# Performance work log

Hardware: AMD Instinct MI355X
Metric: run time of the kernel (lower is better)

Reference implementation:

```python
import jax, jax.numpy as jnp
import numpy as np

N_HEAD = 16

def setup_inputs() -> dict:
    key = jax.random.key(0)
    k1, k2, k3, k4, k5 = jax.random.split(key, 5)
    B, T, C = 2, 2048, 1024
    x = jax.random.normal(k1, (B, T, C), dtype=jnp.float32)
    s = 0.02
    W_attn = jax.random.normal(k2, (C, 3 * C), dtype=jnp.float32) * s
    b_attn = jnp.zeros((3 * C,), dtype=jnp.float32)
    W_proj = jax.random.normal(k3, (C, C), dtype=jnp.float32) * s
    b_proj = jnp.zeros((C,), dtype=jnp.float32)
    return {"x": x, "W_attn": W_attn, "b_attn": b_attn, "W_proj": W_proj, "b_proj": b_proj}

def reference(x, W_attn, b_attn, W_proj, b_proj):
    B, T, C = x.shape
    H = N_HEAD
    hd = C // H
    qkv = x @ W_attn + b_attn                      # (B,T,3C)
    q, k, v = jnp.split(qkv, 3, axis=-1)
    # (B,T,C) -> (B,H,T,hd)
    def to_heads(t):
        return t.reshape(B, T, H, hd).transpose(0, 2, 1, 3)
    q, k, v = to_heads(q), to_heads(k), to_heads(v)
    scale = 1.0 / jnp.sqrt(jnp.asarray(hd, dtype=x.dtype))
    att = jnp.einsum('bhqd,bhkd->bhqk', q, k) * scale  # (B,H,T,T)
    causal = jnp.tril(jnp.ones((T, T), dtype=bool))
    att = jnp.where(causal[None, None], att, -jnp.inf)
    att = jax.nn.softmax(att, axis=-1)
    y = jnp.einsum('bhqk,bhkd->bhqd', att, v)          # (B,H,T,hd)
    y = y.transpose(0, 2, 1, 3).reshape(B, T, C)
    return y @ W_proj + b_proj
```

## Files before the change

kernel.cpp:

```cpp
#include <hip/hip_runtime.h>

#define N_HEAD 16

typedef __attribute__((ext_vector_type(8))) __bf16 bf16x8;
typedef __attribute__((ext_vector_type(8))) short  s16x8;
typedef __attribute__((ext_vector_type(4))) short  s16x4;
typedef __attribute__((ext_vector_type(4))) float  f32x4;
typedef __attribute__((ext_vector_type(4))) unsigned u32x4;

#if __has_builtin(__builtin_amdgcn_exp2f)
#define EXP2(x) __builtin_amdgcn_exp2f(x)
#else
#define EXP2(x) exp2f(x)
#endif
#if __has_builtin(__builtin_amdgcn_rcpf)
#define RCP(x) __builtin_amdgcn_rcpf(x)
#else
#define RCP(x) (1.0f / (x))
#endif

static __device__ __forceinline__ short f2bf(float f) {
    unsigned u = __builtin_bit_cast(unsigned, f);
    unsigned r = (u + 0x7FFFu + ((u >> 16) & 1u)) >> 16;
    return (short)r;
}

static __device__ __forceinline__ unsigned cvt_pk_bf16(float lo, float hi) {
    unsigned d;
    asm("v_cvt_pk_bf16_f32 %0, %1, %2" : "=v"(d) : "v"(lo), "v"(hi));
    return d;
}

static __device__ __forceinline__ void gload_lds16(const void* g, void* l) {
    __builtin_amdgcn_global_load_lds(
        (const __attribute__((address_space(1))) void*)g,
        (__attribute__((address_space(3))) void*)l, 16, 0, 0);
}

__global__ __launch_bounds__(256) void cvt_bf16(
    const float* __restrict__ X, short* __restrict__ Y, int n)
{
    int idx = blockIdx.x * 256 + threadIdx.x;
    size_t base = (size_t)idx * 8;
    if (base + 8 > (size_t)n) return;
    float4 f0 = *(const float4*)&X[base];
    float4 f1 = *(const float4*)&X[base + 4];
    s16x8 o;
    o[0] = f2bf(f0.x); o[1] = f2bf(f0.y); o[2] = f2bf(f0.z); o[3] = f2bf(f0.w);
    o[4] = f2bf(f1.x); o[5] = f2bf(f1.y); o[6] = f2bf(f1.z); o[7] = f2bf(f1.w);
    *(s16x8*)&Y[base] = o;
}

__global__ __launch_bounds__(256) void transpose_w(
    const float* __restrict__ W, short* __restrict__ Wt, int N, int K)
{
    __shared__ short Ts[64][72];
    const int n0 = blockIdx.x * 64, k0 = blockIdx.y * 64;
    const int tid = threadIdx.x;
    const int r = tid >> 4, c4 = (tid & 15) * 4;
#pragma unroll
    for (int i = 0; i < 4; ++i) {
        int row = r + i * 16;
        float4 f = *(const float4*)&W[(size_t)(k0 + row) * N + n0 + c4];
        s16x4 s = { f2bf(f.x), f2bf(f.y), f2bf(f.z), f2bf(f.w) };
        *(s16x4*)&Ts[row][c4] = s;
    }
    __syncthreads();
#pragma unroll
    for (int i = 0; i < 4; ++i) {
        int row = r + i * 16;
        s16x4 s = { Ts[c4 + 0][row], Ts[c4 + 1][row], Ts[c4 + 2][row], Ts[c4 + 3][row] };
        *(s16x4*)&Wt[(size_t)(n0 + row) * K + k0 + c4] = s;
    }
}

__global__ __launch_bounds__(256) void qkv_gemm(
    const short* __restrict__ Xb,
    const short* __restrict__ Wt,
    const float* __restrict__ bias,
    short* __restrict__ Qo, short* __restrict__ Ko, short* __restrict__ Vo)
{
    __shared__ short As[2][128 * 32];
    __shared__ short Bs[2][128 * 32];
    const int tid = threadIdx.x, wave = tid >> 6, lane = tid & 63;
    const int row0 = blockIdx.x * 128, col0 = blockIdx.y * 128;
    const int srow = wave * 16 + (lane >> 2);
    const int scol = (lane & 3) * 8;
    const short* aS = Xb + (size_t)(row0 + srow) * 1024 + scol;
    const short* bS = Wt + (size_t)(col0 + srow) * 1024 + scol;
    const int woff = wave * 512;
    const int wr = (wave >> 1) * 64, wc = (wave & 1) * 64;
    const int arow = lane & 15, ksub = (lane >> 4) * 8;

    f32x4 acc[4][4] = {};

    gload_lds16(aS,             As[0] + woff);
    gload_lds16(aS + 64 * 1024, As[0] + woff + 2048);
    gload_lds16(bS,             Bs[0] + woff);
    gload_lds16(bS + 64 * 1024, Bs[0] + woff + 2048);
    __syncthreads();

    int cur = 0;
    for (int k0 = 0; k0 < 1024; k0 += 32) {
        if (k0 + 32 < 1024) {
            gload_lds16(aS + k0 + 32,             As[cur ^ 1] + woff);
            gload_lds16(aS + k0 + 32 + 64 * 1024, As[cur ^ 1] + woff + 2048);
            gload_lds16(bS + k0 + 32,             Bs[cur ^ 1] + woff);
            gload_lds16(bS + k0 + 32 + 64 * 1024, Bs[cur ^ 1] + woff + 2048);
        }
        bf16x8 af[4], bfr[4];
#pragma unroll
        for (int i = 0; i < 4; ++i) af[i]  = *(const bf16x8*)&As[cur][(wr + i * 16 + arow) * 32 + ksub];
#pragma unroll
        for (int j = 0; j < 4; ++j) bfr[j] = *(const bf16x8*)&Bs[cur][(wc + j * 16 + arow) * 32 + ksub];
#pragma unroll
        for (int i = 0; i < 4; ++i)
#pragma unroll
            for (int j = 0; j < 4; ++j)
                acc[i][j] = __builtin_amdgcn_mfma_f32_16x16x32_bf16(af[i], bfr[j], acc[i][j], 0, 0, 0);
        __syncthreads();
        cur ^= 1;
    }

    const int ccol = lane & 15, crow = (lane >> 4) * 4;
#pragma unroll
    for (int i = 0; i < 4; ++i)
#pragma unroll
        for (int j = 0; j < 4; ++j)
#pragma unroll
            for (int r = 0; r < 4; ++r) {
                int m = row0 + wr + i * 16 + crow + r;
                int n = col0 + wc + j * 16 + ccol;
                float val = acc[i][j][r] + bias[n];
                int which = n >> 10;
                int nc = n & 1023;
                int head = nc >> 6, hd = nc & 63;
                int b = m >> 11, t = m & 2047;
                if (which == 0) {
                    Qo[((size_t)(b * N_HEAD + head) * 2048 + t) * 64 + hd] = f2bf(val * 0.18033688f);
                } else if (which == 1) {
                    Ko[((size_t)(b * N_HEAD + head) * 2048 + t) * 64 + hd] = f2bf(val);
                } else {
                    Vo[((size_t)(b * N_HEAD + head) * 64 + hd) * 2048 + t] = f2bf(val);
                }
            }
}

__global__ __launch_bounds__(256) void attn_kernel(
    const short* __restrict__ Q, const short* __restrict__ K,
    const short* __restrict__ Vt, short* __restrict__ Y)
{
    __shared__ short Ks[2][64 * 64];
    __shared__ short Vs[2][64 * 64];
    const int bh = blockIdx.x;
    const int qt = gridDim.y - 1 - blockIdx.y;
    const int q0 = qt * 64;
    const int b = bh >> 4, h = bh & 15;
    const short* Qh = Q  + (size_t)bh * 2048 * 64;
    const short* Kh = K  + (size_t)bh * 2048 * 64;
    const short* Vh = Vt + (size_t)bh * 64 * 2048;
    const int tid = threadIdx.x, wave = tid >> 6, lane = tid & 63;
    const int qrow0 = q0 + wave * 16;
    const int arow = lane & 15, g = lane >> 4;

    const int rho = wave * 16 + (lane >> 3);
    const int kappa = ((rho >> 5) << 5) | (((rho >> 2) & 3) << 3)
                    | (((rho >> 4) & 1) << 2) | (rho & 3);
    const int xchunk = 8 * ((lane & 7) ^ (rho & 7));
    const short* kSrc = Kh + (size_t)kappa * 64 + xchunk;
    const short* vSrc = Vh + (size_t)rho * 2048 + xchunk;

    bf16x8 qfr[2];
#pragma unroll
    for (int c = 0; c < 2; ++c)
        qfr[c] = *(const bf16x8*)&Qh[(size_t)(qrow0 + arow) * 64 + c * 32 + (g * 8)];

    f32x4 o[4] = {};
    float lsum = 0.f;

    const int nt = qt + 1;

    gload_lds16(kSrc,            Ks[0] + wave * 1024);
    gload_lds16(kSrc + 1024,     Ks[0] + wave * 1024 + 512);
    gload_lds16(vSrc,            Vs[0] + wave * 1024);
    gload_lds16(vSrc + 8 * 2048, Vs[0] + wave * 1024 + 512);
    __syncthreads();

    int cur = 0;
    for (int t = 0; t < nt; ++t) {
        const int kt = t << 6;
        if (t + 1 < nt) {
            const int kn = kt + 64;
            short* kD = Ks[cur ^ 1] + wave * 1024;
            short* vD = Vs[cur ^ 1] + wave * 1024;
            gload_lds16(kSrc + (size_t)kn * 64,        kD);
            gload_lds16(kSrc + (size_t)kn * 64 + 1024, kD + 512);
            gload_lds16(vSrc + kn,                     vD);
            gload_lds16(vSrc + kn + 8 * 2048,          vD + 512);
        }
        if (kt <= qrow0 + 15) {
            const short* Kc = Ks[cur];
            const short* Vc = Vs[cur];
            const bool need_mask = (kt + 64) > qrow0;
            f32x4 s[4] = {};
#pragma unroll
            for (int kc = 0; kc < 4; ++kc) {
                int krow = kc * 16 + arow;
                int xr = krow & 7;
#pragma unroll
                for (int c = 0; c < 2; ++c) {
                    bf16x8 kf = *(const bf16x8*)&Kc[krow * 64 + (((c * 4 + g) ^ xr) * 8)];
                    s[kc] = __builtin_amdgcn_mfma_f32_16x16x32_bf16(kf, qfr[c], s[kc], 0, 0, 0);
                }
            }
            if (need_mask) {
                int q = qrow0 + arow;
#pragma unroll
                for (int kc = 0; kc < 4; ++kc) {
                    int keyb = kt + ((kc >> 1) << 5) + (g << 3) + ((kc & 1) << 2);
#pragma unroll
                    for (int r = 0; r < 4; ++r)
                        if (keyb + r > q) s[kc][r] = -3.0e38f;
                }
            }
            unsigned pa[8];
#pragma unroll
            for (int kc = 0; kc < 4; ++kc) {
                float p0 = EXP2(s[kc][0]);
                float p1 = EXP2(s[kc][1]);
                float p2 = EXP2(s[kc][2]);
                float p3 = EXP2(s[kc][3]);
                lsum += (p0 + p1) + (p2 + p3);
                pa[kc * 2 + 0] = cvt_pk_bf16(p0, p1);
                pa[kc * 2 + 1] = cvt_pk_bf16(p2, p3);
            }
#pragma unroll
            for (int c = 0; c < 2; ++c) {
                bf16x8 pb = __builtin_bit_cast(bf16x8,
                    (u32x4){ pa[4 * c], pa[4 * c + 1], pa[4 * c + 2], pa[4 * c + 3] });
#pragma unroll
                for (int j = 0; j < 4; ++j) {
                    int d = j * 16 + arow;
                    bf16x8 vf = *(const bf16x8*)&Vc[d * 64 + (((c * 4 + g) ^ (d & 7)) * 8)];
                    o[j] = __builtin_amdgcn_mfma_f32_16x16x32_bf16(vf, pb, o[j], 0, 0, 0);
                }
            }
        }
        __syncthreads();
        cur ^= 1;
    }

    {
        float l = lsum;
        l += __shfl_xor(l, 16);
        l += __shfl_xor(l, 32);
        float li = RCP(l);
        int t = qrow0 + arow;
#pragma unroll
        for (int j = 0; j < 4; ++j) {
            s16x4 ov = { f2bf(o[j][0] * li), f2bf(o[j][1] * li),
                         f2bf(o[j][2] * li), f2bf(o[j][3] * li) };
            *(s16x4*)&Y[((size_t)(b * 2048 + t)) * 1024 + h * 64 + j * 16 + 4 * g] = ov;
        }
    }
}

__global__ __launch_bounds__(256) void proj_gemm(
    const short* __restrict__ Yb,
    const short* __restrict__ Wpt,
    const float* __restrict__ bias,
    float* __restrict__ Out)
{
    __shared__ short As[2][128 * 32];
    __shared__ short Bs[2][128 * 32];
    const int tid = threadIdx.x, wave = tid >> 6, lane = tid & 63;
    const int row0 = blockIdx.x * 128, col0 = blockIdx.y * 128;
    const int srow = wave * 16 + (lane >> 2);
    const int scol = (lane & 3) * 8;
    const short* aS = Yb  + (size_t)(row0 + srow) * 1024 + scol;
    const short* bS = Wpt + (size_t)(col0 + srow) * 1024 + scol;
    const int woff = wave * 512;
    const int wr = (wave >> 1) * 64, wc = (wave & 1) * 64;
    const int arow = lane & 15, ksub = (lane >> 4) * 8;

    f32x4 acc[4][4] = {};

    gload_lds16(aS,             As[0] + woff);
    gload_lds16(aS + 64 * 1024, As[0] + woff + 2048);
    gload_lds16(bS,             Bs[0] + woff);
    gload_lds16(bS + 64 * 1024, Bs[0] + woff + 2048);
    __syncthreads();

    int cur = 0;
    for (int k0 = 0; k0 < 1024; k0 += 32) {
        if (k0 + 32 < 1024) {
            gload_lds16(aS + k0 + 32,             As[cur ^ 1] + woff);
            gload_lds16(aS + k0 + 32 + 64 * 1024, As[cur ^ 1] + woff + 2048);
            gload_lds16(bS + k0 + 32,             Bs[cur ^ 1] + woff);
            gload_lds16(bS + k0 + 32 + 64 * 1024, Bs[cur ^ 1] + woff + 2048);
        }
        bf16x8 af[4], bfr[4];
#pragma unroll
        for (int i = 0; i < 4; ++i) af[i]  = *(const bf16x8*)&As[cur][(wr + i * 16 + arow) * 32 + ksub];
#pragma unroll
        for (int j = 0; j < 4; ++j) bfr[j] = *(const bf16x8*)&Bs[cur][(wc + j * 16 + arow) * 32 + ksub];
#pragma unroll
        for (int i = 0; i < 4; ++i)
#pragma unroll
            for (int j = 0; j < 4; ++j)
                acc[i][j] = __builtin_amdgcn_mfma_f32_16x16x32_bf16(af[i], bfr[j], acc[i][j], 0, 0, 0);
        __syncthreads();
        cur ^= 1;
    }

    const int ccol = lane & 15, crow = (lane >> 4) * 4;
#pragma unroll
    for (int i = 0; i < 4; ++i)
#pragma unroll
        for (int j = 0; j < 4; ++j)
#pragma unroll
            for (int r = 0; r < 4; ++r) {
                int m = row0 + wr + i * 16 + crow + r;
                int n = col0 + wc + j * 16 + ccol;
                Out[(size_t)m * 1024 + n] = acc[i][j][r] + bias[n];
            }
}

extern "C" void kernel_launch(void* const* d_in, const int* in_sizes, int n_in,
                              void* d_out, int out_size, void* d_ws, size_t ws_size,
                              hipStream_t stream) {
    const float* x      = (const float*)d_in[0];
    const float* W_attn = (const float*)d_in[1];
    const float* b_attn = (const float*)d_in[2];
    const float* W_proj = (const float*)d_in[3];
    const float* b_proj = (const float*)d_in[4];
    float* out = (float*)d_out;

    short* Xb  = (short*)d_ws;
    short* Wat = Xb + 4194304;
    short* Wpt = Wat + 3145728;
    short* qb  = Wpt + 1048576;
    short* kb  = qb + 4194304;
    short* vb  = kb + 4194304;
    short* yb  = Xb;

    cvt_bf16<<<2048, 256, 0, stream>>>(x, Xb, 4194304);
    transpose_w<<<dim3(48, 16), 256, 0, stream>>>(W_attn, Wat, 3072, 1024);
    transpose_w<<<dim3(16, 16), 256, 0, stream>>>(W_proj, Wpt, 1024, 1024);
    qkv_gemm<<<dim3(32, 24), 256, 0, stream>>>(Xb, Wat, b_attn, qb, kb, vb);
    attn_kernel<<<dim3(32, 32), 256, 0, stream>>>(qb, kb, vb, yb);
    proj_gemm<<<dim3(32, 8), 256, 0, stream>>>(yb, Wpt, b_proj, out);
}
```

Baseline: 115.0 us.

## Rewrite QKV GEMM as 256x256 tile, 8-wave pipelined kernel with swizzled LDS

The QKV projection GEMM now uses 512-thread blocks computing 256x256 output tiles with K-step 64. Global-to-LDS loads are issued in staged quarters interleaved with MFMA phases under explicit barriers, vmcnt waits and s_setprio, and LDS columns are XOR-swizzled to avoid bank conflicts. Block IDs are remapped for L2 locality and the V store is vectorized. This aims at more data reuse and better overlap of memory and compute, at the cost of larger LDS use, high register pressure and a grid of only 192 blocks.

```diff
diff --git a/kernel.cpp b/kernel.cpp
--- a/kernel.cpp
+++ b/kernel.cpp
@@ -36,6 +36,11 @@
         (const __attribute__((address_space(1))) void*)g,
         (__attribute__((address_space(3))) void*)l, 16, 0, 0);
 }
+
+#define BARX() do { asm volatile("" ::: "memory"); __builtin_amdgcn_s_barrier(); \
+                    asm volatile("" ::: "memory"); } while (0)
+#define VMCNT4() asm volatile("s_waitcnt vmcnt(4)" ::: "memory")
+#define VMCNT0() asm volatile("s_waitcnt vmcnt(0)" ::: "memory")
 
 __global__ __launch_bounds__(256) void cvt_bf16(
     const float* __restrict__ X, short* __restrict__ Y, int n)
@@ -74,76 +79,137 @@
     }
 }
 
-__global__ __launch_bounds__(256) void qkv_gemm(
+__global__ __launch_bounds__(512, 1) void qkv_gemm(
     const short* __restrict__ Xb,
     const short* __restrict__ Wt,
     const float* __restrict__ bias,
     short* __restrict__ Qo, short* __restrict__ Ko, short* __restrict__ Vo)
 {
-    __shared__ short As[2][128 * 32];
-    __shared__ short Bs[2][128 * 32];
+    __shared__ short As[2][2][8192];
+    __shared__ short Bs[2][2][8192];
     const int tid = threadIdx.x, wave = tid >> 6, lane = tid & 63;
-    const int row0 = blockIdx.x * 128, col0 = blockIdx.y * 128;
-    const int srow = wave * 16 + (lane >> 2);
-    const int scol = (lane & 3) * 8;
-    const short* aS = Xb + (size_t)(row0 + srow) * 1024 + scol;
-    const short* bS = Wt + (size_t)(col0 + srow) * 1024 + scol;
-    const int woff = wave * 512;
-    const int wr = (wave >> 1) * 64, wc = (wave & 1) * 64;
-    const int arow = lane & 15, ksub = (lane >> 4) * 8;
-
-    f32x4 acc[4][4] = {};
-
-    gload_lds16(aS,             As[0] + woff);
-    gload_lds16(aS + 64 * 1024, As[0] + woff + 2048);
-    gload_lds16(bS,             Bs[0] + woff);
-    gload_lds16(bS + 64 * 1024, Bs[0] + woff + 2048);
-    __syncthreads();
-
-    int cur = 0;
-    for (int k0 = 0; k0 < 1024; k0 += 32) {
-        if (k0 + 32 < 1024) {
-            gload_lds16(aS + k0 + 32,             As[cur ^ 1] + woff);
-            gload_lds16(aS + k0 + 32 + 64 * 1024, As[cur ^ 1] + woff + 2048);
-            gload_lds16(bS + k0 + 32,             Bs[cur ^ 1] + woff);
-            gload_lds16(bS + k0 + 32 + 64 * 1024, Bs[cur ^ 1] + woff + 2048);
-        }
-        bf16x8 af[4], bfr[4];
-#pragma unroll
-        for (int i = 0; i < 4; ++i) af[i]  = *(const bf16x8*)&As[cur][(wr + i * 16 + arow) * 32 + ksub];
-#pragma unroll
-        for (int j = 0; j < 4; ++j) bfr[j] = *(const bf16x8*)&Bs[cur][(wc + j * 16 + arow) * 32 + ksub];
-#pragma unroll
-        for (int i = 0; i < 4; ++i)
-#pragma unroll
-            for (int j = 0; j < 4; ++j)
-                acc[i][j] = __builtin_amdgcn_mfma_f32_16x16x32_bf16(af[i], bfr[j], acc[i][j], 0, 0, 0);
-        __syncthreads();
-        cur ^= 1;
-    }
-
-    const int ccol = lane & 15, crow = (lane >> 4) * 4;
-#pragma unroll
-    for (int i = 0; i < 4; ++i)
-#pragma unroll
-        for (int j = 0; j < 4; ++j)
-#pragma unroll
-            for (int r = 0; r < 4; ++r) {
-                int m = row0 + wr + i * 16 + crow + r;
-                int n = col0 + wc + j * 16 + ccol;
-                float val = acc[i][j][r] + bias[n];
-                int which = n >> 10;
-                int nc = n & 1023;
-                int head = nc >> 6, hd = nc & 63;
-                int b = m >> 11, t = m & 2047;
-                if (which == 0) {
-                    Qo[((size_t)(b * N_HEAD + head) * 2048 + t) * 64 + hd] = f2bf(val * 0.18033688f);
-                } else if (which == 1) {
-                    Ko[((size_t)(b * N_HEAD + head) * 2048 + t) * 64 + hd] = f2bf(val);
-                } else {
-                    Vo[((size_t)(b * N_HEAD + head) * 64 + hd) * 2048 + t] = f2bf(val);
-                }
-            }
+    int bidf = blockIdx.y * 16 + blockIdx.x;
+    bidf = (bidf & 7) * 24 + (bidf >> 3);
+    const int row0 = (bidf % 16) * 256, col0 = (bidf / 16) * 256;
+    const int wm = wave >> 2, wn = wave & 3;
+    const int arow = lane & 15, g = lane >> 4;
+    const int xsw = (arow & 4) << 2;
+    const int aoff0 = (g * 8) ^ xsw;
+    const int aoff1 = (g * 8 + 32) ^ xsw;
+
+    const int srow = tid >> 3;
+    const int sc = ((tid & 7) * 8) ^ (((srow >> 2) & 1) << 4);
+    const short* aBase = Xb + (size_t)(row0 + srow) * 1024 + sc;
+    const short* bBase = Wt + (size_t)(col0 + srow) * 1024 + sc;
+    short* aD = &As[0][0][0] + wave * 512;
+    short* bD = &Bs[0][0][0] + wave * 512;
+
+#define STAGE(t, s) do { const int _b = ((t) & 1) * 16384; const size_t _k = (size_t)(t) * 64; \
+    if ((s) == 0)      { gload_lds16(aBase + _k,          aD + _b);         gload_lds16(aBase + _k + 65536,  aD + _b + 4096); } \
+    else if ((s) == 3) { gload_lds16(aBase + _k + 131072, aD + _b + 8192);  gload_lds16(aBase + _k + 196608, aD + _b + 12288); } \
+    else if ((s) == 1) { gload_lds16(bBase + _k,          bD + _b);         gload_lds16(bBase + _k + 65536,  bD + _b + 4096); } \
+    else               { gload_lds16(bBase + _k + 131072, bD + _b + 8192);  gload_lds16(bBase + _k + 196608, bD + _b + 12288); } \
+} while (0)
+
+    bf16x8 af[4][2], bfr[2][2][2];
+    f32x4 acc[8][4] = {};
+
+#define LDA8(BUF, MH) do { const short* _p = &As[BUF][wm][(MH) * 4096 + arow * 64]; \
+    af[0][0] = *(const bf16x8*)(_p + aoff0);        af[0][1] = *(const bf16x8*)(_p + aoff1); \
+    af[1][0] = *(const bf16x8*)(_p + 1024 + aoff0); af[1][1] = *(const bf16x8*)(_p + 1024 + aoff1); \
+    af[2][0] = *(const bf16x8*)(_p + 2048 + aoff0); af[2][1] = *(const bf16x8*)(_p + 2048 + aoff1); \
+    af[3][0] = *(const bf16x8*)(_p + 3072 + aoff0); af[3][1] = *(const bf16x8*)(_p + 3072 + aoff1); \
+} while (0)
+
+#define LDB4(BUF, NH) do { const short* _p = &Bs[BUF][wn >> 1][(wn & 1) * 4096 + (NH) * 2048 + arow * 64]; \
+    bfr[NH][0][0] = *(const bf16x8*)(_p + aoff0);        bfr[NH][0][1] = *(const bf16x8*)(_p + aoff1); \
+    bfr[NH][1][0] = *(const bf16x8*)(_p + 1024 + aoff0); bfr[NH][1][1] = *(const bf16x8*)(_p + 1024 + aoff1); \
+} while (0)
+
+#define MM(MH, NH, mm, nn) do { \
+    acc[(MH)*4+mm][(NH)*2+nn] = __builtin_amdgcn_mfma_f32_16x16x32_bf16(af[mm][0], bfr[NH][nn][0], acc[(MH)*4+mm][(NH)*2+nn], 0, 0, 0); \
+    acc[(MH)*4+mm][(NH)*2+nn] = __builtin_amdgcn_mfma_f32_16x16x32_bf16(af[mm][1], bfr[NH][nn][1], acc[(MH)*4+mm][(NH)*2+nn], 0, 0, 0); \
+} while (0)
+#define MF16(MH, NH) do { MM(MH,NH,0,0); MM(MH,NH,0,1); MM(MH,NH,1,0); MM(MH,NH,1,1); \
+                          MM(MH,NH,2,0); MM(MH,NH,2,1); MM(MH,NH,3,0); MM(MH,NH,3,1); } while (0)
+
+#define PRIO1() __builtin_amdgcn_s_setprio(1)
+#define PRIO0() __builtin_amdgcn_s_setprio(0)
+
+#define HALFPH(BUF, STa, STb, STc, STd, VM) do { \
+    LDA8(BUF, 0); LDB4(BUF, 0); STa; BARX(); \
+    PRIO1(); MF16(0, 0); PRIO0(); BARX(); \
+    LDB4(BUF, 1); STb; BARX(); \
+    PRIO1(); MF16(0, 1); PRIO0(); BARX(); \
+    LDA8(BUF, 1); STc; BARX(); \
+    PRIO1(); MF16(1, 1); PRIO0(); BARX(); \
+    STd; VM; BARX(); \
+    PRIO1(); MF16(1, 0); PRIO0(); BARX(); \
+} while (0)
+
+    STAGE(0, 0); STAGE(0, 1); STAGE(0, 2); STAGE(0, 3);
+    STAGE(1, 1); STAGE(1, 2);
+    VMCNT4(); BARX();
+
+    for (int i = 0; i < 7; ++i) {
+        HALFPH(0, STAGE(2*i+1, 0), STAGE(2*i+1, 3), STAGE(2*i+2, 1), STAGE(2*i+2, 2), VMCNT4());
+        HALFPH(1, STAGE(2*i+2, 0), STAGE(2*i+2, 3), STAGE(2*i+3, 1), STAGE(2*i+3, 2), VMCNT4());
+    }
+    HALFPH(0, STAGE(15, 0), STAGE(15, 3), ((void)0), ((void)0), VMCNT0());
+    HALFPH(1, ((void)0), ((void)0), ((void)0), ((void)0), VMCNT0());
+
+    const int which = col0 >> 10;
+    const int bb = row0 >> 11;
+    const int nc0 = (col0 & 1023) + wn * 64 + arow;
+    const int t0 = (row0 & 2047) + wm * 128 + g * 4;
+    float bv[4];
+#pragma unroll
+    for (int n = 0; n < 4; ++n) bv[n] = bias[col0 + wn * 64 + n * 16 + arow];
+
+    if (which == 0) {
+#pragma unroll
+        for (int n = 0; n < 4; ++n) {
+            int nc = nc0 + n * 16, head = nc >> 6, hd = nc & 63;
+#pragma unroll
+            for (int m = 0; m < 8; ++m) {
+                size_t tb = (size_t)(bb * N_HEAD + head) * 2048 + t0 + m * 16;
+#pragma unroll
+                for (int r = 0; r < 4; ++r)
+                    Qo[(tb + r) * 64 + hd] = f2bf((acc[m][n][r] + bv[n]) * 0.18033688f);
+            }
+        }
+    } else if (which == 1) {
+#pragma unroll
+        for (int n = 0; n < 4; ++n) {
+            int nc = nc0 + n * 16, head = nc >> 6, hd = nc & 63;
+#pragma unroll
+            for (int m = 0; m < 8; ++m) {
+                size_t tb = (size_t)(bb * N_HEAD + head) * 2048 + t0 + m * 16;
+#pragma unroll
+                for (int r = 0; r < 4; ++r)
+                    Ko[(tb + r) * 64 + hd] = f2bf(acc[m][n][r] + bv[n]);
+            }
+        }
+    } else {
+#pragma unroll
+        for (int n = 0; n < 4; ++n) {
+            int nc = nc0 + n * 16, head = nc >> 6, hd = nc & 63;
+#pragma unroll
+            for (int m = 0; m < 8; ++m) {
+                s16x4 ov = { f2bf(acc[m][n][0] + bv[n]), f2bf(acc[m][n][1] + bv[n]),
+                             f2bf(acc[m][n][2] + bv[n]), f2bf(acc[m][n][3] + bv[n]) };
+                *(s16x4*)&Vo[((size_t)(bb * N_HEAD + head) * 64 + hd) * 2048 + t0 + m * 16] = ov;
+            }
+        }
+    }
+#undef STAGE
+#undef LDA8
+#undef LDB4
+#undef MM
+#undef MF16
+#undef HALFPH
+#undef PRIO1
+#undef PRIO0
 }
 
 __global__ __launch_bounds__(256) void attn_kernel(
@@ -271,8 +337,8 @@
     const float* __restrict__ bias,
     float* __restrict__ Out)
 {
-    __shared__ short As[2][128 * 32];
-    __shared__ short Bs[2][128 * 32];
+    __shared__ short As2[2][128 * 32];
+    __shared__ short Bs2[2][128 * 32];
     const int tid = threadIdx.x, wave = tid >> 6, lane = tid & 63;
     const int row0 = blockIdx.x * 128, col0 = blockIdx.y * 128;
     const int srow = wave * 16 + (lane >> 2);
@@ -285,25 +351,25 @@
 
     f32x4 acc[4][4] = {};
 
-    gload_lds16(aS,             As[0] + woff);
-    gload_lds16(aS + 64 * 1024, As[0] + woff + 2048);
-    gload_lds16(bS,             Bs[0] + woff);
-    gload_lds16(bS + 64 * 1024, Bs[0] + woff + 2048);
+    gload_lds16(aS,             As2[0] + woff);
+    gload_lds16(aS + 64 * 1024, As2[0] + woff + 2048);
+    gload_lds16(bS,             Bs2[0] + woff);
+    gload_lds16(bS + 64 * 1024, Bs2[0] + woff + 2048);
     __syncthreads();
 
     int cur = 0;
     for (int k0 = 0; k0 < 1024; k0 += 32) {
         if (k0 + 32 < 1024) {
-            gload_lds16(aS + k0 + 32,             As[cur ^ 1] + woff);
-            gload_lds16(aS + k0 + 32 + 64 * 1024, As[cur ^ 1] + woff + 2048);
-            gload_lds16(bS + k0 + 32,             Bs[cur ^ 1] + woff);
-            gload_lds16(bS + k0 + 32 + 64 * 1024, Bs[cur ^ 1] + woff + 2048);
+            gload_lds16(aS + k0 + 32,             As2[cur ^ 1] + woff);
+            gload_lds16(aS + k0 + 32 + 64 * 1024, As2[cur ^ 1] + woff + 2048);
+            gload_lds16(bS + k0 + 32,             Bs2[cur ^ 1] + woff);
+            gload_lds16(bS + k0 + 32 + 64 * 1024, Bs2[cur ^ 1] + woff + 2048);
         }
         bf16x8 af[4], bfr[4];
 #pragma unroll
-        for (int i = 0; i < 4; ++i) af[i]  = *(const bf16x8*)&As[cur][(wr + i * 16 + arow) * 32 + ksub];
-#pragma unroll
-        for (int j = 0; j < 4; ++j) bfr[j] = *(const bf16x8*)&Bs[cur][(wc + j * 16 + arow) * 32 + ksub];
+        for (int i = 0; i < 4; ++i) af[i]  = *(const bf16x8*)&As2[cur][(wr + i * 16 + arow) * 32 + ksub];
+#pragma unroll
+        for (int j = 0; j < 4; ++j) bfr[j] = *(const bf16x8*)&Bs2[cur][(wc + j * 16 + arow) * 32 + ksub];
 #pragma unroll
         for (int i = 0; i < 4; ++i)
 #pragma unroll
@@ -347,7 +413,7 @@
     cvt_bf16<<<2048, 256, 0, stream>>>(x, Xb, 4194304);
     transpose_w<<<dim3(48, 16), 256, 0, stream>>>(W_attn, Wat, 3072, 1024);
     transpose_w<<<dim3(16, 16), 256, 0, stream>>>(W_proj, Wpt, 1024, 1024);
-    qkv_gemm<<<dim3(32, 24), 256, 0, stream>>>(Xb, Wat, b_attn, qb, kb, vb);
+    qkv_gemm<<<dim3(16, 12), 512, 0, stream>>>(Xb, Wat, b_attn, qb, kb, vb);
     attn_kernel<<<dim3(32, 32), 256, 0, stream>>>(qb, kb, vb, yb);
     proj_gemm<<<dim3(32, 8), 256, 0, stream>>>(yb, Wpt, b_proj, out);
 }
```

New measurement: 118.0 us. +2.7%, slower.

## Triple-buffer GEMM LDS staging with swizzled layout and vmcnt-based waits

Applied to the files above, without the earlier changes.

Both GEMM kernels move from double to triple buffering, keeping two tiles in flight and waiting with explicit s_waitcnt vmcnt(4) plus a raw barrier instead of a full __syncthreads drain. The K-chunk position within each LDS row is XOR-swizzled on the global-to-LDS copy and matched on the fragment reads, to reduce LDS bank conflicts. The QKV epilogue hoists the Q/K/V choice and bias load out of the inner loops and writes V in 4-element vector stores. LDS use grows by half, which may lower occupancy, and correctness depends on the hand-counted vmcnt values.

```diff
diff --git a/kernel.cpp b/kernel.cpp
--- a/kernel.cpp
+++ b/kernel.cpp
@@ -37,6 +37,11 @@
         (__attribute__((address_space(3))) void*)l, 16, 0, 0);
 }
 
+#define BARX() do { asm volatile("" ::: "memory"); __builtin_amdgcn_s_barrier(); \
+                    asm volatile("" ::: "memory"); } while (0)
+#define VMCNT4() asm volatile("s_waitcnt vmcnt(4)" ::: "memory")
+#define VMCNT0() asm volatile("s_waitcnt vmcnt(0)" ::: "memory")
+
 __global__ __launch_bounds__(256) void cvt_bf16(
     const float* __restrict__ X, short* __restrict__ Y, int n)
 {
@@ -80,70 +85,94 @@
     const float* __restrict__ bias,
     short* __restrict__ Qo, short* __restrict__ Ko, short* __restrict__ Vo)
 {
-    __shared__ short As[2][128 * 32];
-    __shared__ short Bs[2][128 * 32];
+    __shared__ short As[3 * 4096];
+    __shared__ short Bs[3 * 4096];
     const int tid = threadIdx.x, wave = tid >> 6, lane = tid & 63;
     const int row0 = blockIdx.x * 128, col0 = blockIdx.y * 128;
     const int srow = wave * 16 + (lane >> 2);
-    const int scol = (lane & 3) * 8;
-    const short* aS = Xb + (size_t)(row0 + srow) * 1024 + scol;
-    const short* bS = Wt + (size_t)(col0 + srow) * 1024 + scol;
+    const int sc = (((lane & 3) ^ ((lane >> 3) & 3)) * 8);
+    const short* aS = Xb + (size_t)(row0 + srow) * 1024 + sc;
+    const short* bS = Wt + (size_t)(col0 + srow) * 1024 + sc;
     const int woff = wave * 512;
     const int wr = (wave >> 1) * 64, wc = (wave & 1) * 64;
-    const int arow = lane & 15, ksub = (lane >> 4) * 8;
+    const int arow = lane & 15, g = lane >> 4;
+    const int foff = (g ^ ((arow >> 1) & 3)) * 8;
 
     f32x4 acc[4][4] = {};
 
-    gload_lds16(aS,             As[0] + woff);
-    gload_lds16(aS + 64 * 1024, As[0] + woff + 2048);
-    gload_lds16(bS,             Bs[0] + woff);
-    gload_lds16(bS + 64 * 1024, Bs[0] + woff + 2048);
-    __syncthreads();
+#define STAGE(T, BUF) do { const size_t _k = (size_t)(T) * 32; \
+    gload_lds16(aS + _k,             As + (BUF) * 4096 + woff); \
+    gload_lds16(aS + _k + 64 * 1024, As + (BUF) * 4096 + woff + 2048); \
+    gload_lds16(bS + _k,             Bs + (BUF) * 4096 + woff); \
+    gload_lds16(bS + _k + 64 * 1024, Bs + (BUF) * 4096 + woff + 2048); \
+} while (0)
+
+#define COMPUTE(BUF) do { \
+    bf16x8 af[4], bfr[4]; \
+    _Pragma("unroll") \
+    for (int i = 0; i < 4; ++i) af[i]  = *(const bf16x8*)&As[(BUF) * 4096 + (wr + i * 16 + arow) * 32 + foff]; \
+    _Pragma("unroll") \
+    for (int j = 0; j < 4; ++j) bfr[j] = *(const bf16x8*)&Bs[(BUF) * 4096 + (wc + j * 16 + arow) * 32 + foff]; \
+    _Pragma("unroll") \
+    for (int i = 0; i < 4; ++i) \
+        _Pragma("unroll") \
+        for (int j = 0; j < 4; ++j) \
+            acc[i][j] = __builtin_amdgcn_mfma_f32_16x16x32_bf16(af[i], bfr[j], acc[i][j], 0, 0, 0); \
+} while (0)
+
+    STAGE(0, 0); STAGE(1, 1);
+    VMCNT4(); BARX();
 
     int cur = 0;
-    for (int k0 = 0; k0 < 1024; k0 += 32) {
-        if (k0 + 32 < 1024) {
-            gload_lds16(aS + k0 + 32,             As[cur ^ 1] + woff);
-            gload_lds16(aS + k0 + 32 + 64 * 1024, As[cur ^ 1] + woff + 2048);
-            gload_lds16(bS + k0 + 32,             Bs[cur ^ 1] + woff);
-            gload_lds16(bS + k0 + 32 + 64 * 1024, Bs[cur ^ 1] + woff + 2048);
+    for (int t = 0; t < 30; ++t) {
+        int nbuf = cur + 2; if (nbuf >= 3) nbuf -= 3;
+        STAGE(t + 2, nbuf);
+        COMPUTE(cur);
+        VMCNT4(); BARX();
+        cur = (cur == 2) ? 0 : cur + 1;
+    }
+    COMPUTE(cur); VMCNT0(); BARX();
+    cur = (cur == 2) ? 0 : cur + 1;
+    COMPUTE(cur);
+#undef STAGE
+#undef COMPUTE
+
+    const int which = col0 >> 10;
+    const int bb = row0 >> 11;
+    const int ccol = arow, crow = g * 4;
+#pragma unroll
+    for (int j = 0; j < 4; ++j) {
+        int n = col0 + wc + j * 16 + ccol;
+        float bv = bias[n];
+        int nc = n & 1023, head = nc >> 6, hd = nc & 63;
+        if (which == 0) {
+#pragma unroll
+            for (int i = 0; i < 4; ++i) {
+                int t0 = (row0 & 2047) + wr + i * 16 + crow;
+#pragma unroll
+                for (int r = 0; r < 4; ++r)
+                    Qo[((size_t)(bb * N_HEAD + head) * 2048 + t0 + r) * 64 + hd] =
+                        f2bf((acc[i][j][r] + bv) * 0.18033688f);
+            }
+        } else if (which == 1) {
+#pragma unroll
+            for (int i = 0; i < 4; ++i) {
+                int t0 = (row0 & 2047) + wr + i * 16 + crow;
+#pragma unroll
+                for (int r = 0; r < 4; ++r)
+                    Ko[((size_t)(bb * N_HEAD + head) * 2048 + t0 + r) * 64 + hd] =
+                        f2bf(acc[i][j][r] + bv);
+            }
+        } else {
+#pragma unroll
+            for (int i = 0; i < 4; ++i) {
+                int t0 = (row0 & 2047) + wr + i * 16 + crow;
+                s16x4 ov = { f2bf(acc[i][j][0] + bv), f2bf(acc[i][j][1] + bv),
+                             f2bf(acc[i][j][2] + bv), f2bf(acc[i][j][3] + bv) };
+                *(s16x4*)&Vo[((size_t)(bb * N_HEAD + head) * 64 + hd) * 2048 + t0] = ov;
+            }
         }
-        bf16x8 af[4], bfr[4];
-#pragma unroll
-        for (int i = 0; i < 4; ++i) af[i]  = *(const bf16x8*)&As[cur][(wr + i * 16 + arow) * 32 + ksub];
-#pragma unroll
-        for (int j = 0; j < 4; ++j) bfr[j] = *(const bf16x8*)&Bs[cur][(wc + j * 16 + arow) * 32 + ksub];
-#pragma unroll
-        for (int i = 0; i < 4; ++i)
-#pragma unroll
-            for (int j = 0; j < 4; ++j)
-                acc[i][j] = __builtin_amdgcn_mfma_f32_16x16x32_bf16(af[i], bfr[j], acc[i][j], 0, 0, 0);
-        __syncthreads();
-        cur ^= 1;
-    }
-
-    const int ccol = lane & 15, crow = (lane >> 4) * 4;
-#pragma unroll
-    for (int i = 0; i < 4; ++i)
-#pragma unroll
-        for (int j = 0; j < 4; ++j)
-#pragma unroll
-            for (int r = 0; r < 4; ++r) {
-                int m = row0 + wr + i * 16 + crow + r;
-                int n = col0 + wc + j * 16 + ccol;
-                float val = acc[i][j][r] + bias[n];
-                int which = n >> 10;
-                int nc = n & 1023;
-                int head = nc >> 6, hd = nc & 63;
-                int b = m >> 11, t = m & 2047;
-                if (which == 0) {
-                    Qo[((size_t)(b * N_HEAD + head) * 2048 + t) * 64 + hd] = f2bf(val * 0.18033688f);
-                } else if (which == 1) {
-                    Ko[((size_t)(b * N_HEAD + head) * 2048 + t) * 64 + hd] = f2bf(val);
-                } else {
-                    Vo[((size_t)(b * N_HEAD + head) * 64 + hd) * 2048 + t] = f2bf(val);
-                }
-            }
+    }
 }
 
 __global__ __launch_bounds__(256) void attn_kernel(
@@ -271,49 +300,59 @@
     const float* __restrict__ bias,
     float* __restrict__ Out)
 {
-    __shared__ short As[2][128 * 32];
-    __shared__ short Bs[2][128 * 32];
+    __shared__ short As[3 * 4096];
+    __shared__ short Bs[3 * 4096];
     const int tid = threadIdx.x, wave = tid >> 6, lane = tid & 63;
     const int row0 = blockIdx.x * 128, col0 = blockIdx.y * 128;
     const int srow = wave * 16 + (lane >> 2);
-    const int scol = (lane & 3) * 8;
-    const short* aS = Yb  + (size_t)(row0 + srow) * 1024 + scol;
-    const short* bS = Wpt + (size_t)(col0 + srow) * 1024 + scol;
+    const int sc = (((lane & 3) ^ ((lane >> 3) & 3)) * 8);
+    const short* aS = Yb  + (size_t)(row0 + srow) * 1024 + sc;
+    const short* bS = Wpt + (size_t)(col0 + srow) * 1024 + sc;
     const int woff = wave * 512;
     const int wr = (wave >> 1) * 64, wc = (wave & 1) * 64;
-    const int arow = lane & 15, ksub = (lane >> 4) * 8;
+    const int arow = lane & 15, g = lane >> 4;
+    const int foff = (g ^ ((arow >> 1) & 3)) * 8;
 
     f32x4 acc[4][4] = {};
 
-    gload_lds16(aS,             As[0] + woff);
-    gload_lds16(aS + 64 * 1024, As[0] + woff + 2048);
-    gload_lds16(bS,             Bs[0] + woff);
-    gload_lds16(bS + 64 * 1024, Bs[0] + woff + 2048);
-    __syncthreads();
+#define STAGE(T, BUF) do { const size_t _k = (size_t)(T) * 32; \
+    gload_lds16(aS + _k,             As + (BUF) * 4096 + woff); \
+    gload_lds16(aS + _k + 64 * 1024, As + (BUF) * 4096 + woff + 2048); \
+    gload_lds16(bS + _k,             Bs + (BUF) * 4096 + woff); \
+    gload_lds16(bS + _k + 64 * 1024, Bs + (BUF) * 4096 + woff + 2048); \
+} while (0)
+
+#define COMPUTE(BUF) do { \
+    bf16x8 af[4], bfr[4]; \
+    _Pragma("unroll") \
+    for (int i = 0; i < 4; ++i) af[i]  = *(const bf16x8*)&As[(BUF) * 4096 + (wr + i * 16 + arow) * 32 + foff]; \
+    _Pragma("unroll") \
+    for (int j = 0; j < 4; ++j) bfr[j] = *(const bf16x8*)&Bs[(BUF) * 4096 + (wc + j * 16 + arow) * 32 + foff]; \
+    _Pragma("unroll") \
+    for (int i = 0; i < 4; ++i) \
+        _Pragma("unroll") \
+        for (int j = 0; j < 4; ++j) \
+            acc[i][j] = __builtin_amdgcn_mfma_f32_16x16x32_bf16(af[i], bfr[j], acc[i][j], 0, 0, 0); \
+} while (0)
+
+    STAGE(0, 0); STAGE(1, 1);
+    VMCNT4(); BARX();
 
     int cur = 0;
-    for (int k0 = 0; k0 < 1024; k0 += 32) {
-        if (k0 + 32 < 1024) {
-            gload_lds16(aS + k0 + 32,             As[cur ^ 1] + woff);
-            gload_lds16(aS + k0 + 32 + 64 * 1024, As[cur ^ 1] + woff + 2048);
-            gload_lds16(bS + k0 + 32,             Bs[cur ^ 1] + woff);
-            gload_lds16(bS + k0 + 32 + 64 * 1024, Bs[cur ^ 1] + woff + 2048);
-        }
-        bf16x8 af[4], bfr[4];
-#pragma unroll
-        for (int i = 0; i < 4; ++i) af[i]  = *(const bf16x8*)&As[cur][(wr + i * 16 + arow) * 32 + ksub];
-#pragma unroll
-        for (int j = 0; j < 4; ++j) bfr[j] = *(const bf16x8*)&Bs[cur][(wc + j * 16 + arow) * 32 + ksub];
-#pragma unroll
-        for (int i = 0; i < 4; ++i)
-#pragma unroll
-            for (int j = 0; j < 4; ++j)
-                acc[i][j] = __builtin_amdgcn_mfma_f32_16x16x32_bf16(af[i], bfr[j], acc[i][j], 0, 0, 0);
-        __syncthreads();
-        cur ^= 1;
-    }
-
-    const int ccol = lane & 15, crow = (lane >> 4) * 4;
+    for (int t = 0; t < 30; ++t) {
+        int nbuf = cur + 2; if (nbuf >= 3) nbuf -= 3;
+        STAGE(t + 2, nbuf);
+        COMPUTE(cur);
+        VMCNT4(); BARX();
+        cur = (cur == 2) ? 0 : cur + 1;
+    }
+    COMPUTE(cur); VMCNT0(); BARX();
+    cur = (cur == 2) ? 0 : cur + 1;
+    COMPUTE(cur);
+#undef STAGE
+#undef COMPUTE
+
+    const int ccol = arow, crow = g * 4;
 #pragma unroll
     for (int i = 0; i < 4; ++i)
 #pragma unroll
```

Measured after the change: 118.2 us. 2.8% more time.
